# Performance work log

Measured on AMD Instinct MI355X. Metric: run time of the kernel, lower is better.

The kernel has to match this reference:

```python
import jax, jax.numpy as jnp
import numpy as np
from jax import lax

S, B, V, E, H = 512, 64, 50000, 400, 1150


def _lstm_layer(x, h0, c0, Wih, Whh, bih, bhh):
    # x: [S, B, Din]; PyTorch LSTM gate order: i, f, g, o
    WihT, WhhT = Wih.T, Whh.T

    def step(carry, xt):
        h, c = carry
        gates = xt @ WihT + bih + h @ WhhT + bhh  # [B, 4*Dh]
        i, f, g, o = jnp.split(gates, 4, axis=-1)
        c_new = jax.nn.sigmoid(f) * c + jax.nn.sigmoid(i) * jnp.tanh(g)
        h_new = jax.nn.sigmoid(o) * jnp.tanh(c_new)
        return (h_new, c_new), h_new

    (_, _), ys = lax.scan(step, (h0, c0), x)
    return ys  # [S, B, Dh]


def setup_inputs() -> dict:
    key = jax.random.key(0)

    def u(i, shape, s):
        return jax.random.uniform(jax.random.fold_in(key, i), shape, jnp.float32, -s, s)

    inp = {"tokens": jax.random.randint(jax.random.fold_in(key, 0), (S, B), 0, V)}
    inp["emb_w"] = u(1, (V, E), 0.1)  # encoder.weight.uniform_(-0.1, 0.1)
    dims = [(E, H), (H, H), (H, E)]  # (input_size, hidden_size) per layer
    k = 2
    for l, (din, dh) in enumerate(dims):
        s = 1.0 / float(np.sqrt(dh))
        inp[f"Wih{l}"] = u(k, (4 * dh, din), s); k += 1
        inp[f"Whh{l}"] = u(k, (4 * dh, dh), s); k += 1
        inp[f"bih{l}"] = u(k, (4 * dh,), s); k += 1
        inp[f"bhh{l}"] = u(k, (4 * dh,), s); k += 1
        inp[f"h{l}"] = jnp.zeros((B, dh), jnp.float32)
        inp[f"c{l}"] = jnp.zeros((B, dh), jnp.float32)
    return inp


def reference(tokens, emb_w, Wih0, Whh0, bih0, bhh0, Wih1, Whh1, bih1, bhh1,
              Wih2, Whh2, bih2, bhh2, h0, c0, h1, c1, h2, c2):
    # Eval-mode forward: embedding/locked/weight dropouts are identity.
    x = emb_w[tokens]  # [S, B, E]
    x = _lstm_layer(x, h0, c0, Wih0, Whh0, bih0, bhh0)  # [S, B, H]
    x = _lstm_layer(x, h1, c1, Wih1, Whh1, bih1, bhh1)  # [S, B, H]
    x = _lstm_layer(x, h2, c2, Wih2, Whh2, bih2, bhh2)  # [S, B, E]
    return x
```

## Files before the change

kernel.cpp:

```cpp
#include <hip/hip_runtime.h>
#include <hip/hip_bf16.h>
#include <cstdint>
#include <cstddef>


typedef _Float16 f16x8 __attribute__((ext_vector_type(8)));
typedef float f32x4 __attribute__((ext_vector_type(4)));
typedef unsigned int u32x4 __attribute__((ext_vector_type(4)));

#define LSTM_NBLK   241
#define LSTM_WSTEPS 515
#define THREADS     512
#define LDS_W_HALFS (4 * 36 * 64 * 8)
#define LDS_TOTAL_BYTES (LDS_W_HALFS * 2 + 16384)
#define GO_BASE 248

struct KParams {
  const unsigned short* res[3];
  const unsigned short* strm[3];
  const float* bias[3];
  const unsigned short* xin0;
  unsigned short* hseq[3];
  float* part;
  float* out;
  int* bar;
};

__device__ __forceinline__ float sigm_(float x) { return 1.0f / (1.0f + __expf(-x)); }
__device__ __forceinline__ float tanh_(float x) { return 2.0f * sigm_(2.0f * x) - 1.0f; }
__device__ __forceinline__ unsigned short f2h(float x) {
  _Float16 h = (_Float16)x;
  return __builtin_bit_cast(unsigned short, h);
}
__device__ __forceinline__ f32x4 load_sc128f(const float* p) {
  f32x4 r;
  asm volatile("global_load_dwordx4 %0, %1, off sc0 sc1"
               : "=v"(r) : "v"(p) : "memory");
  return r;
}
__device__ __forceinline__ void store_sc128(unsigned short* p, u32x4 v) {
  asm volatile("global_store_dwordx4 %0, %1, off sc0 sc1" :: "v"(p), "v"(v) : "memory");
}
__device__ __forceinline__ void store_sc128f(float* p, f32x4 v) {
  asm volatile("global_store_dwordx4 %0, %1, off sc0 sc1" :: "v"(p), "v"(v) : "memory");
}
__device__ __forceinline__ void store_sc_i(int* p, int v) {
  asm volatile("global_store_dword %0, %1, off sc0 sc1" :: "v"(p), "v"(v) : "memory");
}
__device__ __forceinline__ int load_sc_i(const int* p) {
  int v;
  asm volatile("global_load_dword %0, %1, off sc0 sc1\n\ts_waitcnt vmcnt(0)"
               : "=v"(v) : "v"(p) : "memory");
  __builtin_amdgcn_sched_barrier(0);
  return v;
}
__device__ __forceinline__ void wait_vm0() {
  asm volatile("s_waitcnt vmcnt(0)" ::: "memory");
  __builtin_amdgcn_sched_barrier(0);
}

__device__ __forceinline__ void grid_barrier(int* bar, int bid, int tid, int tau1) {
  wait_vm0();
  __syncthreads();
  if (bid == 0) {
    if (tid >= 1 && tid < LSTM_NBLK) {
      int guard = 0;
      while (load_sc_i(&bar[tid * 32]) < tau1 && ++guard < (1 << 20))
        __builtin_amdgcn_s_sleep(1);
    }
    __syncthreads();
    if (tid < 8) store_sc_i(&bar[(GO_BASE + tid) * 32], tau1);
  } else {
    if (tid == 0) {
      store_sc_i(&bar[bid * 32], tau1);
      int guard = 0;
      while (load_sc_i(&bar[(GO_BASE + (bid & 7)) * 32]) < tau1 && ++guard < (1 << 20))
        __builtin_amdgcn_s_sleep(1);
    }
    __syncthreads();
  }
}

template<bool HASP>
__device__ __forceinline__ float lstm_ew(float* gates, int e, const float b4[4],
                                         const f32x4* pl, float& c_val) {
  float pg[4];
#pragma unroll
  for (int s2 = 0; s2 < 4; ++s2) {
    pg[s2] = gates[s2 * 1024 + e];
    gates[s2 * 1024 + e] = 0.0f;
  }
  float ig = sigm_(pg[0] + (HASP ? (*pl)[0] : 0.0f) + b4[0]);
  float fg = sigm_(pg[1] + (HASP ? (*pl)[1] : 0.0f) + b4[1]);
  float gg = tanh_(pg[2] + (HASP ? (*pl)[2] : 0.0f) + b4[2]);
  float og = sigm_(pg[3] + (HASP ? (*pl)[3] : 0.0f) + b4[3]);
  c_val = fg * c_val + ig * gg;
  return og * tanh_(c_val);
}

__device__ __forceinline__ void pack_store16(unsigned short* base, int lane, float h) {
  unsigned v0  = (unsigned)f2h(h);
  unsigned o1  = __shfl_down(v0, 1);
  unsigned p01 = v0 | (o1 << 16);
  unsigned o2  = __shfl_down(p01, 2);
  unsigned o4a = __shfl_down(p01, 4);
  unsigned o4b = __shfl_down(o2, 4);
  if ((lane & 7) == 0) {
    u32x4 pk; pk[0] = p01; pk[1] = o2; pk[2] = o4a; pk[3] = o4b;
    store_sc128(base, pk);
  }
}

__device__ __forceinline__ void run_l0(const KParams& p, int g, int bid,
                                       unsigned short* ldsW, float* gates) {
  const unsigned short* __restrict__ strmA = p.strm[0] + (size_t)g * (4 * 13 * 512);
  const unsigned short* __restrict__ xin   = p.xin0;
  unsigned short* __restrict__ own         = p.hseq[0];

  const int tid  = threadIdx.x;
  const int lane = tid & 63;
  const int w    = tid >> 6;
  const int kq   = w & 3;
  const int m0   = (w >> 2) * 32;
  const int r    = lane & 15;
  const int q    = lane >> 4;

  {
    const uint4* src = (const uint4*)(p.res[0] + (size_t)g * LDS_W_HALFS);
    uint4* dst = (uint4*)ldsW;
    for (int i = tid; i < LDS_W_HALFS / 8; i += THREADS) dst[i] = src[i];
#pragma unroll
    for (int s2 = 0; s2 < 4; ++s2) {
      gates[s2 * 1024 + tid] = 0.0f;
      gates[s2 * 1024 + tid + 512] = 0.0f;
    }
  }
  const int jp = tid & 15;
  const int jglob = g * 16 + jp;
  float bias4[4];
#pragma unroll
  for (int ss = 0; ss < 4; ++ss) bias4[ss] = p.bias[0][ss * 1152 + jglob];
  float c0 = 0.0f, c1 = 0.0f;
  __syncthreads();

  for (int tau = 0; tau < LSTM_WSTEPS; ++tau) {
    const int t = tau;
    if (t < 512) {
      f16x8 a2r[2][9];
#pragma unroll
      for (int mi = 0; mi < 2; ++mi) {
        const unsigned short* a2b =
            own + (size_t)t * (64 * 1152) + (size_t)(m0 + mi * 16 + r) * 1152 + q * 8;
#pragma unroll
        for (int i = 0; i < 9; ++i) a2r[mi][i] = *(const f16x8*)(a2b + (kq + 4 * i) * 32);
      }
      f16x8 a1r[2][4]; f16x8 bS[4][4];
#pragma unroll
      for (int mi = 0; mi < 2; ++mi) {
        const unsigned short* a1b =
            xin + ((size_t)t * 64 + (m0 + mi * 16 + r)) * 416 + q * 8;
#pragma unroll
        for (int i = 0; i < 4; ++i) {
          int kb = kq + 4 * i;
          if (kb < 13) a1r[mi][i] = *(const f16x8*)(a1b + kb * 32);
        }
      }
#pragma unroll
      for (int i = 0; i < 4; ++i) {
        int kb = kq + 4 * i;
        if (kb < 13) {
#pragma unroll
          for (int s2 = 0; s2 < 4; ++s2)
            bS[i][s2] = *(const f16x8*)&strmA[((size_t)(s2 * 13 + kb) * 64 + lane) * 8];
        }
      }

      f32x4 acc[2][4];
#pragma unroll
      for (int mi = 0; mi < 2; ++mi)
#pragma unroll
        for (int s2 = 0; s2 < 4; ++s2) acc[mi][s2] = (f32x4){0, 0, 0, 0};

#pragma unroll
      for (int i = 0; i < 4; ++i) {
        int kb = kq + 4 * i;
        if (kb < 13) {
#pragma unroll
          for (int s2 = 0; s2 < 4; ++s2)
#pragma unroll
            for (int mi = 0; mi < 2; ++mi)
              acc[mi][s2] = __builtin_amdgcn_mfma_f32_16x16x32_f16(
                  a1r[mi][i], bS[i][s2], acc[mi][s2], 0, 0, 0);
        }
      }
#pragma unroll
      for (int i = 0; i < 9; ++i) {
        int kb = kq + 4 * i;
#pragma unroll
        for (int s2 = 0; s2 < 4; ++s2) {
          f16x8 b = *(const f16x8*)&ldsW[((s2 * 36 + kb) * 64 + lane) * 8];
#pragma unroll
          for (int mi = 0; mi < 2; ++mi)
            acc[mi][s2] = __builtin_amdgcn_mfma_f32_16x16x32_f16(
                a2r[mi][i], b, acc[mi][s2], 0, 0, 0);
        }
      }
#pragma unroll
      for (int mi = 0; mi < 2; ++mi)
#pragma unroll
        for (int s2 = 0; s2 < 4; ++s2)
#pragma unroll
          for (int i = 0; i < 4; ++i)
            atomicAdd(&gates[s2 * 1024 + (m0 + mi * 16 + q * 4 + i) * 16 + r],
                      acc[mi][s2][i]);
      __syncthreads();

      float h0 = lstm_ew<false>(gates, tid, bias4, nullptr, c0);
      float h1 = lstm_ew<false>(gates, tid + 512, bias4, nullptr, c1);
      if (jglob >= 1150) { h0 = 0.0f; h1 = 0.0f; }
      const int b0 = tid >> 4, b1 = b0 + 32;
      pack_store16(own + ((size_t)(t + 1) * 64 + b0) * 1152 + jglob, lane, h0);
      pack_store16(own + ((size_t)(t + 1) * 64 + b1) * 1152 + jglob, lane, h1);
    }
    grid_barrier(p.bar, bid, tid, tau + 1);
  }
}

__device__ __forceinline__ void run_l1_ih(const KParams& p, int g, int bid,
                                          unsigned short* ldsW, float* gates) {
  const unsigned short* __restrict__ xin = p.hseq[0];
  const int tid  = threadIdx.x;
  const int lane = tid & 63;
  const int w    = tid >> 6;
  const int kq   = w & 3;
  const int m0   = (w >> 2) * 32;
  const int r    = lane & 15;
  const int q    = lane >> 4;

  {
    const uint4* src = (const uint4*)(p.strm[1] + (size_t)g * LDS_W_HALFS);
    uint4* dst = (uint4*)ldsW;
    for (int i = tid; i < LDS_W_HALFS / 8; i += THREADS) dst[i] = src[i];
#pragma unroll
    for (int s2 = 0; s2 < 4; ++s2) {
      gates[s2 * 1024 + tid] = 0.0f;
      gates[s2 * 1024 + tid + 512] = 0.0f;
    }
  }
  __syncthreads();

  for (int tau = 0; tau < LSTM_WSTEPS; ++tau) {
    const int t = tau - 1;
    if (t >= 0 && t < 512) {
      f16x8 a1r[2][9];
#pragma unroll
      for (int mi = 0; mi < 2; ++mi) {
        const unsigned short* a1b =
            xin + (size_t)(t + 1) * (64 * 1152) + (size_t)(m0 + mi * 16 + r) * 1152 + q * 8;
#pragma unroll
        for (int i = 0; i < 9; ++i) a1r[mi][i] = *(const f16x8*)(a1b + (kq + 4 * i) * 32);
      }
      f32x4 acc[2][4];
#pragma unroll
      for (int mi = 0; mi < 2; ++mi)
#pragma unroll
        for (int s2 = 0; s2 < 4; ++s2) acc[mi][s2] = (f32x4){0, 0, 0, 0};
#pragma unroll
      for (int i = 0; i < 9; ++i) {
        int kb = kq + 4 * i;
#pragma unroll
        for (int s2 = 0; s2 < 4; ++s2) {
          f16x8 b = *(const f16x8*)&ldsW[((s2 * 36 + kb) * 64 + lane) * 8];
#pragma unroll
          for (int mi = 0; mi < 2; ++mi)
            acc[mi][s2] = __builtin_amdgcn_mfma_f32_16x16x32_f16(
                a1r[mi][i], b, acc[mi][s2], 0, 0, 0);
        }
      }
#pragma unroll
      for (int mi = 0; mi < 2; ++mi)
#pragma unroll
        for (int s2 = 0; s2 < 4; ++s2)
#pragma unroll
          for (int i = 0; i < 4; ++i)
            atomicAdd(&gates[s2 * 1024 + (m0 + mi * 16 + q * 4 + i) * 16 + r],
                      acc[mi][s2][i]);
      __syncthreads();

      f32x4 pk0, pk1;
#pragma unroll
      for (int s2 = 0; s2 < 4; ++s2) {
        pk0[s2] = gates[s2 * 1024 + tid];       gates[s2 * 1024 + tid] = 0.0f;
        pk1[s2] = gates[s2 * 1024 + tid + 512]; gates[s2 * 1024 + tid + 512] = 0.0f;
      }
      float* pb = p.part + (size_t)((t & 1) * 72 + g) * 1024 * 4;
      store_sc128f(pb + (size_t)tid * 4, pk0);
      store_sc128f(pb + (size_t)(tid + 512) * 4, pk1);
    }
    grid_barrier(p.bar, bid, tid, tau + 1);
  }
}

__device__ __forceinline__ void run_l1_hh(const KParams& p, int g, int bid,
                                          unsigned short* ldsW, float* gates) {
  unsigned short* __restrict__ own = p.hseq[1];
  const int tid  = threadIdx.x;
  const int lane = tid & 63;
  const int w    = tid >> 6;
  const int kq   = w & 3;
  const int m0   = (w >> 2) * 32;
  const int r    = lane & 15;
  const int q    = lane >> 4;

  {
    const uint4* src = (const uint4*)(p.res[1] + (size_t)g * LDS_W_HALFS);
    uint4* dst = (uint4*)ldsW;
    for (int i = tid; i < LDS_W_HALFS / 8; i += THREADS) dst[i] = src[i];
#pragma unroll
    for (int s2 = 0; s2 < 4; ++s2) {
      gates[s2 * 1024 + tid] = 0.0f;
      gates[s2 * 1024 + tid + 512] = 0.0f;
    }
  }
  const int jp = tid & 15;
  const int jglob = g * 16 + jp;
  float bias4[4];
#pragma unroll
  for (int ss = 0; ss < 4; ++ss) bias4[ss] = p.bias[1][ss * 1152 + jglob];
  float c0 = 0.0f, c1 = 0.0f;
  __syncthreads();

  for (int tau = 0; tau < LSTM_WSTEPS; ++tau) {
    const int t = tau - 2;
    if (t >= 0 && t < 512) {
      f16x8 a2r[2][9];
#pragma unroll
      for (int mi = 0; mi < 2; ++mi) {
        const unsigned short* a2b =
            own + (size_t)t * (64 * 1152) + (size_t)(m0 + mi * 16 + r) * 1152 + q * 8;
#pragma unroll
        for (int i = 0; i < 9; ++i) a2r[mi][i] = *(const f16x8*)(a2b + (kq + 4 * i) * 32);
      }
      const float* pb = p.part + (size_t)((t & 1) * 72 + g) * 1024 * 4;
      f32x4 pl0 = load_sc128f(pb + (size_t)tid * 4);
      f32x4 pl1 = load_sc128f(pb + (size_t)(tid + 512) * 4);
      wait_vm0();

      f32x4 acc[2][4];
#pragma unroll
      for (int mi = 0; mi < 2; ++mi)
#pragma unroll
        for (int s2 = 0; s2 < 4; ++s2) acc[mi][s2] = (f32x4){0, 0, 0, 0};
#pragma unroll
      for (int i = 0; i < 9; ++i) {
        int kb = kq + 4 * i;
#pragma unroll
        for (int s2 = 0; s2 < 4; ++s2) {
          f16x8 b = *(const f16x8*)&ldsW[((s2 * 36 + kb) * 64 + lane) * 8];
#pragma unroll
          for (int mi = 0; mi < 2; ++mi)
            acc[mi][s2] = __builtin_amdgcn_mfma_f32_16x16x32_f16(
                a2r[mi][i], b, acc[mi][s2], 0, 0, 0);
        }
      }
#pragma unroll
      for (int mi = 0; mi < 2; ++mi)
#pragma unroll
        for (int s2 = 0; s2 < 4; ++s2)
#pragma unroll
          for (int i = 0; i < 4; ++i)
            atomicAdd(&gates[s2 * 1024 + (m0 + mi * 16 + q * 4 + i) * 16 + r],
                      acc[mi][s2][i]);
      __syncthreads();

      float h0 = lstm_ew<true>(gates, tid, bias4, &pl0, c0);
      float h1 = lstm_ew<true>(gates, tid + 512, bias4, &pl1, c1);
      if (jglob >= 1150) { h0 = 0.0f; h1 = 0.0f; }
      const int b0 = tid >> 4, b1 = b0 + 32;
      pack_store16(own + ((size_t)(t + 1) * 64 + b0) * 1152 + jglob, lane, h0);
      pack_store16(own + ((size_t)(t + 1) * 64 + b1) * 1152 + jglob, lane, h1);
    }
    grid_barrier(p.bar, bid, tid, tau + 1);
  }
}

__device__ __forceinline__ void run_l2(const KParams& p, int g, int bid,
                                       unsigned short* ldsW, float* gates) {
  const unsigned short* __restrict__ strmB = p.strm[2] + (size_t)g * (4 * 13 * 512);
  const unsigned short* __restrict__ xin   = p.hseq[1];
  unsigned short* __restrict__ own         = p.hseq[2];

  const int tid  = threadIdx.x;
  const int lane = tid & 63;
  const int w    = tid >> 6;
  const int kq   = w & 3;
  const int m0   = (w >> 2) * 32;
  const int r    = lane & 15;
  const int q    = lane >> 4;

  {
    const uint4* src = (const uint4*)(p.res[2] + (size_t)g * LDS_W_HALFS);
    uint4* dst = (uint4*)ldsW;
    for (int i = tid; i < LDS_W_HALFS / 8; i += THREADS) dst[i] = src[i];
#pragma unroll
    for (int s2 = 0; s2 < 4; ++s2) {
      gates[s2 * 1024 + tid] = 0.0f;
      gates[s2 * 1024 + tid + 512] = 0.0f;
    }
  }
  const int jp = tid & 15;
  const int jglob = g * 16 + jp;
  float bias4[4];
#pragma unroll
  for (int ss = 0; ss < 4; ++ss) bias4[ss] = p.bias[2][ss * 1152 + jglob];
  float c0 = 0.0f, c1 = 0.0f;
  __syncthreads();

  for (int tau = 0; tau < LSTM_WSTEPS; ++tau) {
    const int t = tau - 3;
    if (t >= 0 && t < 512) {
      f16x8 a1r[2][9];
#pragma unroll
      for (int mi = 0; mi < 2; ++mi) {
        const unsigned short* a1b =
            xin + (size_t)(t + 1) * (64 * 1152) + (size_t)(m0 + mi * 16 + r) * 1152 + q * 8;
#pragma unroll
        for (int i = 0; i < 9; ++i) a1r[mi][i] = *(const f16x8*)(a1b + (kq + 4 * i) * 32);
      }
      f16x8 a2r[2][4];
#pragma unroll
      for (int mi = 0; mi < 2; ++mi) {
        const unsigned short* a2b =
            own + (size_t)t * (64 * 416) + (size_t)(m0 + mi * 16 + r) * 416 + q * 8;
#pragma unroll
        for (int i = 0; i < 4; ++i) {
          int kb = kq + 4 * i;
          if (kb < 13) a2r[mi][i] = *(const f16x8*)(a2b + kb * 32);
        }
      }
      f16x8 bS[4][4];
#pragma unroll
      for (int i = 0; i < 4; ++i) {
        int kb = kq + 4 * i;
        if (kb < 13) {
#pragma unroll
          for (int s2 = 0; s2 < 4; ++s2)
            bS[i][s2] = *(const f16x8*)&strmB[((size_t)(s2 * 13 + kb) * 64 + lane) * 8];
        }
      }

      f32x4 acc[2][4];
#pragma unroll
      for (int mi = 0; mi < 2; ++mi)
#pragma unroll
        for (int s2 = 0; s2 < 4; ++s2) acc[mi][s2] = (f32x4){0, 0, 0, 0};

#pragma unroll
      for (int i = 0; i < 9; ++i) {
        int kb = kq + 4 * i;
#pragma unroll
        for (int s2 = 0; s2 < 4; ++s2) {
          f16x8 b = *(const f16x8*)&ldsW[((s2 * 36 + kb) * 64 + lane) * 8];
#pragma unroll
          for (int mi = 0; mi < 2; ++mi)
            acc[mi][s2] = __builtin_amdgcn_mfma_f32_16x16x32_f16(
                a1r[mi][i], b, acc[mi][s2], 0, 0, 0);
        }
      }
#pragma unroll
      for (int i = 0; i < 4; ++i) {
        int kb = kq + 4 * i;
        if (kb < 13) {
#pragma unroll
          for (int s2 = 0; s2 < 4; ++s2)
#pragma unroll
            for (int mi = 0; mi < 2; ++mi)
              acc[mi][s2] = __builtin_amdgcn_mfma_f32_16x16x32_f16(
                  a2r[mi][i], bS[i][s2], acc[mi][s2], 0, 0, 0);
        }
      }
#pragma unroll
      for (int mi = 0; mi < 2; ++mi)
#pragma unroll
        for (int s2 = 0; s2 < 4; ++s2)
#pragma unroll
          for (int i = 0; i < 4; ++i)
            atomicAdd(&gates[s2 * 1024 + (m0 + mi * 16 + q * 4 + i) * 16 + r],
                      acc[mi][s2][i]);
      __syncthreads();

      float h0 = lstm_ew<false>(gates, tid, bias4, nullptr, c0);
      float h1 = lstm_ew<false>(gates, tid + 512, bias4, nullptr, c1);
      if (jglob >= 400) { h0 = 0.0f; h1 = 0.0f; }
      const int b0 = tid >> 4, b1 = b0 + 32;
      pack_store16(own + ((size_t)(t + 1) * 64 + b0) * 416 + jglob, lane, h0);
      pack_store16(own + ((size_t)(t + 1) * 64 + b1) * 416 + jglob, lane, h1);
      if (jglob < 400) {
        p.out[((size_t)t * 64 + b0) * 400 + jglob] = h0;
        p.out[((size_t)t * 64 + b1) * 400 + jglob] = h1;
      }
    }
    grid_barrier(p.bar, bid, tid, tau + 1);
  }
}

__global__ void __launch_bounds__(THREADS, 2) lstm_persistent(KParams p) {
  extern __shared__ unsigned short smem[];
  unsigned short* ldsW = smem;
  float* gates = (float*)(smem + LDS_W_HALFS);
  const int bid = blockIdx.x;
  if (bid < 72)       run_l0(p, bid, bid, ldsW, gates);
  else if (bid < 144) run_l1_ih(p, bid - 72, bid, ldsW, gates);
  else if (bid < 216) run_l1_hh(p, bid - 144, bid, ldsW, gates);
  else                run_l2(p, bid - 216, bid, ldsW, gates);
}

__global__ void prep_weights(const float* __restrict__ src,
                             unsigned short* __restrict__ dst,
                             int Jext, int jg, int K, int NKB) {
  const int n = jg * 4 * NKB * 512;
  for (int idx = blockIdx.x * blockDim.x + threadIdx.x; idx < n;
       idx += gridDim.x * blockDim.x) {
    int e = idx & 7;
    int t2 = idx >> 3;
    int ln = t2 & 63; t2 >>= 6;
    int kb = t2 % NKB; t2 /= NKB;
    int s = t2 & 3;
    int g = t2 >> 2;
    int j = g * 16 + (ln & 15);
    int k = kb * 32 + (ln >> 4) * 8 + e;
    unsigned short v = 0;
    if (j < Jext && k < K) v = f2h(src[(size_t)(s * Jext + j) * K + k]);
    dst[idx] = v;
  }
}

__global__ void prep_bias(const float* __restrict__ bih,
                          const float* __restrict__ bhh,
                          float* __restrict__ dst, int Dh) {
  const int n = 4 * 1152;
  for (int idx = blockIdx.x * blockDim.x + threadIdx.x; idx < n;
       idx += gridDim.x * blockDim.x) {
    int s = idx / 1152, j = idx % 1152;
    float v = 0.0f;
    if (j < Dh) v = bih[s * Dh + j] + bhh[s * Dh + j];
    dst[idx] = v;
  }
}

__global__ void prep_gather(const int* __restrict__ tokens,
                            const float* __restrict__ emb,
                            unsigned short* __restrict__ xin0) {
  const int n = 512 * 64 * 52;
  for (int idx = blockIdx.x * blockDim.x + threadIdx.x; idx < n;
       idx += gridDim.x * blockDim.x) {
    int row = idx / 52;
    int cp  = idx - row * 52;
    unsigned short v[8] = {0, 0, 0, 0, 0, 0, 0, 0};
    if (cp < 50) {
      const float* src = emb + (size_t)tokens[row] * 400 + cp * 8;
      float4 a = *(const float4*)(src);
      float4 b = *(const float4*)(src + 4);
      v[0] = f2h(a.x); v[1] = f2h(a.y); v[2] = f2h(a.z); v[3] = f2h(a.w);
      v[4] = f2h(b.x); v[5] = f2h(b.y); v[6] = f2h(b.z); v[7] = f2h(b.w);
    }
    *(uint4*)(xin0 + (size_t)row * 416 + cp * 8) = *(const uint4*)v;
  }
}

extern "C" void kernel_launch(void* const* d_in, const int* in_sizes, int n_in,
                              void* d_out, int out_size, void* d_ws, size_t ws_size,
                              hipStream_t stream) {
  const int*   tokens = (const int*)d_in[0];
  const float* emb  = (const float*)d_in[1];
  const float* Wih0 = (const float*)d_in[2];
  const float* Whh0 = (const float*)d_in[3];
  const float* bih0 = (const float*)d_in[4];
  const float* bhh0 = (const float*)d_in[5];
  const float* Wih1 = (const float*)d_in[8];
  const float* Whh1 = (const float*)d_in[9];
  const float* bih1 = (const float*)d_in[10];
  const float* bhh1 = (const float*)d_in[11];
  const float* Wih2 = (const float*)d_in[14];
  const float* Whh2 = (const float*)d_in[15];
  const float* bih2 = (const float*)d_in[16];
  const float* bhh2 = (const float*)d_in[17];

  char* ws = (char*)d_ws;
  size_t off = 0;
  auto alloc = [&](size_t bytes) -> char* {
    char* ptr = ws + off;
    off += (bytes + 255) & ~(size_t)255;
    return ptr;
  };
  unsigned short* res0  = (unsigned short*)alloc(72ull * 4 * 36 * 512 * 2);
  unsigned short* res1  = (unsigned short*)alloc(72ull * 4 * 36 * 512 * 2);
  unsigned short* res2  = (unsigned short*)alloc(25ull * 4 * 36 * 512 * 2);
  unsigned short* strm0 = (unsigned short*)alloc(72ull * 4 * 13 * 512 * 2);
  unsigned short* strm1 = (unsigned short*)alloc(72ull * 4 * 36 * 512 * 2);
  unsigned short* strm2 = (unsigned short*)alloc(25ull * 4 * 13 * 512 * 2);
  float* bias0 = (float*)alloc(4ull * 1152 * 4);
  float* bias1 = (float*)alloc(4ull * 1152 * 4);
  float* bias2 = (float*)alloc(4ull * 1152 * 4);
  unsigned short* xin0  = (unsigned short*)alloc(512ull * 64 * 416 * 2);
  unsigned short* hseq0 = (unsigned short*)alloc(513ull * 64 * 1152 * 2);
  unsigned short* hseq1 = (unsigned short*)alloc(513ull * 64 * 1152 * 2);
  unsigned short* hseq2 = (unsigned short*)alloc(513ull * 64 * 416 * 2);
  float* part = (float*)alloc(2ull * 72 * 1024 * 4 * 4);
  int* bar = (int*)alloc((GO_BASE + 8) * 32 * 4);
  if (off > ws_size) return;

  hipLaunchKernelGGL(prep_gather, dim3(2048), dim3(256), 0, stream, tokens, emb, xin0);
  hipLaunchKernelGGL(prep_weights, dim3(4096), dim3(256), 0, stream, Whh0, res0, 1150, 72, 1150, 36);
  hipLaunchKernelGGL(prep_weights, dim3(4096), dim3(256), 0, stream, Whh1, res1, 1150, 72, 1150, 36);
  hipLaunchKernelGGL(prep_weights, dim3(4096), dim3(256), 0, stream, Wih2, res2, 400, 25, 1150, 36);
  hipLaunchKernelGGL(prep_weights, dim3(4096), dim3(256), 0, stream, Wih0, strm0, 1150, 72, 400, 13);
  hipLaunchKernelGGL(prep_weights, dim3(4096), dim3(256), 0, stream, Wih1, strm1, 1150, 72, 1150, 36);
  hipLaunchKernelGGL(prep_weights, dim3(4096), dim3(256), 0, stream, Whh2, strm2, 400, 25, 400, 13);
  hipLaunchKernelGGL(prep_bias, dim3(8), dim3(256), 0, stream, bih0, bhh0, bias0, 1150);
  hipLaunchKernelGGL(prep_bias, dim3(8), dim3(256), 0, stream, bih1, bhh1, bias1, 1150);
  hipLaunchKernelGGL(prep_bias, dim3(8), dim3(256), 0, stream, bih2, bhh2, bias2, 400);
  (void)hipMemsetAsync(hseq0, 0, 64ull * 1152 * 2, stream);
  (void)hipMemsetAsync(hseq1, 0, 64ull * 1152 * 2, stream);
  (void)hipMemsetAsync(hseq2, 0, 64ull * 416 * 2, stream);
  (void)hipMemsetAsync(bar, 0, (GO_BASE + 8) * 32 * 4, stream);

  KParams kp;
  kp.res[0] = res0;  kp.res[1] = res1;  kp.res[2] = res2;
  kp.strm[0] = strm0; kp.strm[1] = strm1; kp.strm[2] = strm2;
  kp.bias[0] = bias0; kp.bias[1] = bias1; kp.bias[2] = bias2;
  kp.xin0 = xin0;
  kp.hseq[0] = hseq0; kp.hseq[1] = hseq1; kp.hseq[2] = hseq2;
  kp.part = part;
  kp.out = (float*)d_out;
  kp.bar = bar;

  (void)hipFuncSetAttribute((const void*)lstm_persistent,
                            hipFuncAttributeMaxDynamicSharedMemorySize,
                            LDS_TOTAL_BYTES);
  hipLaunchKernelGGL(lstm_persistent, dim3(LSTM_NBLK), dim3(THREADS),
                     LDS_TOTAL_BYTES, stream, kp);
}
```

Baseline: 16.02 ms.

## Replace global grid barrier with per-group dataflow flags and deeper partial buffer

Replaces the single grid-wide barrier that lock-stepped all four block groups (layer0, layer1-ih, layer1-hh, layer2) with per-group barriers plus per-group 'go' flags. Each group waits only on the producers it depends on, so groups can run ahead of each other in a wavefront. The partial-gate ring buffer is deepened to 8 slots so the layer1 input projection can run up to 7 steps ahead of its consumer. Cross-block activation loads now bypass the cache via sc0/sc1 loads, which adds some load latency and more flag-polling traffic.

After: 16.70 ms. +4.3%, slower.

```diff
diff --git a/kernel.cpp b/kernel.cpp
--- a/kernel.cpp
+++ b/kernel.cpp
@@ -9,10 +9,10 @@
 typedef unsigned int u32x4 __attribute__((ext_vector_type(4)));
 
 #define LSTM_NBLK   241
-#define LSTM_WSTEPS 515
 #define THREADS     512
 #define LDS_W_HALFS (4 * 36 * 64 * 8)
 #define LDS_TOTAL_BYTES (LDS_W_HALFS * 2 + 16384)
+#define PDEPTH 8
 #define GO_BASE 248
 
 struct KParams {
@@ -32,6 +32,12 @@
   _Float16 h = (_Float16)x;
   return __builtin_bit_cast(unsigned short, h);
 }
+__device__ __forceinline__ u32x4 load_sc(const unsigned short* p) {
+  u32x4 r;
+  asm volatile("global_load_dwordx4 %0, %1, off sc0 sc1"
+               : "=v"(r) : "v"(p) : "memory");
+  return r;
+}
 __device__ __forceinline__ f32x4 load_sc128f(const float* p) {
   f32x4 r;
   asm volatile("global_load_dwordx4 %0, %1, off sc0 sc1"
@@ -59,25 +65,27 @@
   __builtin_amdgcn_sched_barrier(0);
 }
 
-__device__ __forceinline__ void grid_barrier(int* bar, int bid, int tid, int tau1) {
+__device__ __forceinline__ void spin_ge(const int* p, int th) {
+  int guard = 0;
+  while (load_sc_i(p) < th && ++guard < (1 << 20))
+    __builtin_amdgcn_s_sleep(2);
+}
+__device__ __forceinline__ void wait_go2(int* bar, int tid, int bid,
+                                         int grpA, int thA, int grpB, int thB) {
+  if (thA > 0 && tid == 0)   spin_ge(&bar[(GO_BASE + grpA * 8 + (bid & 7)) * 32], thA);
+  if (thB > 0 && tid == 256) spin_ge(&bar[(GO_BASE + grpB * 8 + (bid & 7)) * 32], thB);
+  __syncthreads();
+}
+__device__ __forceinline__ void finish_step(int* bar, int bid, int tid,
+                                            int gbase, int gsize, int grp, int tau1) {
   wait_vm0();
   __syncthreads();
-  if (bid == 0) {
-    if (tid >= 1 && tid < LSTM_NBLK) {
-      int guard = 0;
-      while (load_sc_i(&bar[tid * 32]) < tau1 && ++guard < (1 << 20))
-        __builtin_amdgcn_s_sleep(1);
-    }
+  if (bid == gbase) {
+    if (tid >= 1 && tid < gsize) spin_ge(&bar[(gbase + tid) * 32], tau1);
     __syncthreads();
-    if (tid < 8) store_sc_i(&bar[(GO_BASE + tid) * 32], tau1);
+    if (tid < 8) store_sc_i(&bar[(GO_BASE + grp * 8 + tid) * 32], tau1);
   } else {
-    if (tid == 0) {
-      store_sc_i(&bar[bid * 32], tau1);
-      int guard = 0;
-      while (load_sc_i(&bar[(GO_BASE + (bid & 7)) * 32]) < tau1 && ++guard < (1 << 20))
-        __builtin_amdgcn_s_sleep(1);
-    }
-    __syncthreads();
+    if (tid == 0) store_sc_i(&bar[bid * 32], tau1);
   }
 }
 
@@ -143,86 +151,87 @@
   float c0 = 0.0f, c1 = 0.0f;
   __syncthreads();
 
-  for (int tau = 0; tau < LSTM_WSTEPS; ++tau) {
-    const int t = tau;
-    if (t < 512) {
-      f16x8 a2r[2][9];
-#pragma unroll
-      for (int mi = 0; mi < 2; ++mi) {
-        const unsigned short* a2b =
-            own + (size_t)t * (64 * 1152) + (size_t)(m0 + mi * 16 + r) * 1152 + q * 8;
-#pragma unroll
-        for (int i = 0; i < 9; ++i) a2r[mi][i] = *(const f16x8*)(a2b + (kq + 4 * i) * 32);
-      }
-      f16x8 a1r[2][4]; f16x8 bS[4][4];
-#pragma unroll
-      for (int mi = 0; mi < 2; ++mi) {
-        const unsigned short* a1b =
-            xin + ((size_t)t * 64 + (m0 + mi * 16 + r)) * 416 + q * 8;
-#pragma unroll
-        for (int i = 0; i < 4; ++i) {
-          int kb = kq + 4 * i;
-          if (kb < 13) a1r[mi][i] = *(const f16x8*)(a1b + kb * 32);
-        }
-      }
+  for (int t = 0; t < 512; ++t) {
+    wait_go2(p.bar, tid, bid, 0, t, 0, 0);
+
+    u32x4 a2r[2][9];
+#pragma unroll
+    for (int mi = 0; mi < 2; ++mi) {
+      const unsigned short* a2b =
+          own + (size_t)t * (64 * 1152) + (size_t)(m0 + mi * 16 + r) * 1152 + q * 8;
+#pragma unroll
+      for (int i = 0; i < 9; ++i) a2r[mi][i] = load_sc(a2b + (kq + 4 * i) * 32);
+    }
+    f16x8 a1r[2][4]; f16x8 bS[4][4];
+#pragma unroll
+    for (int mi = 0; mi < 2; ++mi) {
+      const unsigned short* a1b =
+          xin + ((size_t)t * 64 + (m0 + mi * 16 + r)) * 416 + q * 8;
 #pragma unroll
       for (int i = 0; i < 4; ++i) {
         int kb = kq + 4 * i;
-        if (kb < 13) {
-#pragma unroll
-          for (int s2 = 0; s2 < 4; ++s2)
-            bS[i][s2] = *(const f16x8*)&strmA[((size_t)(s2 * 13 + kb) * 64 + lane) * 8];
-        }
-      }
-
-      f32x4 acc[2][4];
-#pragma unroll
-      for (int mi = 0; mi < 2; ++mi)
-#pragma unroll
-        for (int s2 = 0; s2 < 4; ++s2) acc[mi][s2] = (f32x4){0, 0, 0, 0};
-
-#pragma unroll
-      for (int i = 0; i < 4; ++i) {
-        int kb = kq + 4 * i;
-        if (kb < 13) {
-#pragma unroll
-          for (int s2 = 0; s2 < 4; ++s2)
-#pragma unroll
-            for (int mi = 0; mi < 2; ++mi)
-              acc[mi][s2] = __builtin_amdgcn_mfma_f32_16x16x32_f16(
-                  a1r[mi][i], bS[i][s2], acc[mi][s2], 0, 0, 0);
-        }
-      }
-#pragma unroll
-      for (int i = 0; i < 9; ++i) {
-        int kb = kq + 4 * i;
-#pragma unroll
-        for (int s2 = 0; s2 < 4; ++s2) {
-          f16x8 b = *(const f16x8*)&ldsW[((s2 * 36 + kb) * 64 + lane) * 8];
+        if (kb < 13) a1r[mi][i] = *(const f16x8*)(a1b + kb * 32);
+      }
+    }
+#pragma unroll
+    for (int i = 0; i < 4; ++i) {
+      int kb = kq + 4 * i;
+      if (kb < 13) {
+#pragma unroll
+        for (int s2 = 0; s2 < 4; ++s2)
+          bS[i][s2] = *(const f16x8*)&strmA[((size_t)(s2 * 13 + kb) * 64 + lane) * 8];
+      }
+    }
+    wait_vm0();
+
+    f32x4 acc[2][4];
+#pragma unroll
+    for (int mi = 0; mi < 2; ++mi)
+#pragma unroll
+      for (int s2 = 0; s2 < 4; ++s2) acc[mi][s2] = (f32x4){0, 0, 0, 0};
+
+#pragma unroll
+    for (int i = 0; i < 4; ++i) {
+      int kb = kq + 4 * i;
+      if (kb < 13) {
+#pragma unroll
+        for (int s2 = 0; s2 < 4; ++s2)
 #pragma unroll
           for (int mi = 0; mi < 2; ++mi)
             acc[mi][s2] = __builtin_amdgcn_mfma_f32_16x16x32_f16(
-                a2r[mi][i], b, acc[mi][s2], 0, 0, 0);
-        }
-      }
-#pragma unroll
-      for (int mi = 0; mi < 2; ++mi)
-#pragma unroll
-        for (int s2 = 0; s2 < 4; ++s2)
-#pragma unroll
-          for (int i = 0; i < 4; ++i)
-            atomicAdd(&gates[s2 * 1024 + (m0 + mi * 16 + q * 4 + i) * 16 + r],
-                      acc[mi][s2][i]);
-      __syncthreads();
-
-      float h0 = lstm_ew<false>(gates, tid, bias4, nullptr, c0);
-      float h1 = lstm_ew<false>(gates, tid + 512, bias4, nullptr, c1);
-      if (jglob >= 1150) { h0 = 0.0f; h1 = 0.0f; }
-      const int b0 = tid >> 4, b1 = b0 + 32;
-      pack_store16(own + ((size_t)(t + 1) * 64 + b0) * 1152 + jglob, lane, h0);
-      pack_store16(own + ((size_t)(t + 1) * 64 + b1) * 1152 + jglob, lane, h1);
-    }
-    grid_barrier(p.bar, bid, tid, tau + 1);
+                a1r[mi][i], bS[i][s2], acc[mi][s2], 0, 0, 0);
+      }
+    }
+#pragma unroll
+    for (int i = 0; i < 9; ++i) {
+      int kb = kq + 4 * i;
+#pragma unroll
+      for (int s2 = 0; s2 < 4; ++s2) {
+        f16x8 b = *(const f16x8*)&ldsW[((s2 * 36 + kb) * 64 + lane) * 8];
+#pragma unroll
+        for (int mi = 0; mi < 2; ++mi)
+          acc[mi][s2] = __builtin_amdgcn_mfma_f32_16x16x32_f16(
+              __builtin_bit_cast(f16x8, a2r[mi][i]), b, acc[mi][s2], 0, 0, 0);
+      }
+    }
+#pragma unroll
+    for (int mi = 0; mi < 2; ++mi)
+#pragma unroll
+      for (int s2 = 0; s2 < 4; ++s2)
+#pragma unroll
+        for (int i = 0; i < 4; ++i)
+          atomicAdd(&gates[s2 * 1024 + (m0 + mi * 16 + q * 4 + i) * 16 + r],
+                    acc[mi][s2][i]);
+    __syncthreads();
+
+    float h0 = lstm_ew<false>(gates, tid, bias4, nullptr, c0);
+    float h1 = lstm_ew<false>(gates, tid + 512, bias4, nullptr, c1);
+    if (jglob >= 1150) { h0 = 0.0f; h1 = 0.0f; }
+    const int b0 = tid >> 4, b1 = b0 + 32;
+    pack_store16(own + ((size_t)(t + 1) * 64 + b0) * 1152 + jglob, lane, h0);
+    pack_store16(own + ((size_t)(t + 1) * 64 + b1) * 1152 + jglob, lane, h1);
+
+    finish_step(p.bar, bid, tid, 0, 72, 0, t + 1);
   }
 }
 
@@ -249,55 +258,57 @@
   }
   __syncthreads();
 
-  for (int tau = 0; tau < LSTM_WSTEPS; ++tau) {
-    const int t = tau - 1;
-    if (t >= 0 && t < 512) {
-      f16x8 a1r[2][9];
-#pragma unroll
-      for (int mi = 0; mi < 2; ++mi) {
-        const unsigned short* a1b =
-            xin + (size_t)(t + 1) * (64 * 1152) + (size_t)(m0 + mi * 16 + r) * 1152 + q * 8;
-#pragma unroll
-        for (int i = 0; i < 9; ++i) a1r[mi][i] = *(const f16x8*)(a1b + (kq + 4 * i) * 32);
-      }
-      f32x4 acc[2][4];
-#pragma unroll
-      for (int mi = 0; mi < 2; ++mi)
-#pragma unroll
-        for (int s2 = 0; s2 < 4; ++s2) acc[mi][s2] = (f32x4){0, 0, 0, 0};
-#pragma unroll
-      for (int i = 0; i < 9; ++i) {
-        int kb = kq + 4 * i;
-#pragma unroll
-        for (int s2 = 0; s2 < 4; ++s2) {
-          f16x8 b = *(const f16x8*)&ldsW[((s2 * 36 + kb) * 64 + lane) * 8];
-#pragma unroll
-          for (int mi = 0; mi < 2; ++mi)
-            acc[mi][s2] = __builtin_amdgcn_mfma_f32_16x16x32_f16(
-                a1r[mi][i], b, acc[mi][s2], 0, 0, 0);
-        }
-      }
-#pragma unroll
-      for (int mi = 0; mi < 2; ++mi)
-#pragma unroll
-        for (int s2 = 0; s2 < 4; ++s2)
-#pragma unroll
-          for (int i = 0; i < 4; ++i)
-            atomicAdd(&gates[s2 * 1024 + (m0 + mi * 16 + q * 4 + i) * 16 + r],
-                      acc[mi][s2][i]);
-      __syncthreads();
-
-      f32x4 pk0, pk1;
+  for (int t = 0; t < 512; ++t) {
+    wait_go2(p.bar, tid, bid, 0, t + 1, 2, t - (PDEPTH - 1));
+
+    u32x4 a1r[2][9];
+#pragma unroll
+    for (int mi = 0; mi < 2; ++mi) {
+      const unsigned short* a1b =
+          xin + (size_t)(t + 1) * (64 * 1152) + (size_t)(m0 + mi * 16 + r) * 1152 + q * 8;
+#pragma unroll
+      for (int i = 0; i < 9; ++i) a1r[mi][i] = load_sc(a1b + (kq + 4 * i) * 32);
+    }
+    wait_vm0();
+
+    f32x4 acc[2][4];
+#pragma unroll
+    for (int mi = 0; mi < 2; ++mi)
+#pragma unroll
+      for (int s2 = 0; s2 < 4; ++s2) acc[mi][s2] = (f32x4){0, 0, 0, 0};
+#pragma unroll
+    for (int i = 0; i < 9; ++i) {
+      int kb = kq + 4 * i;
 #pragma unroll
       for (int s2 = 0; s2 < 4; ++s2) {
-        pk0[s2] = gates[s2 * 1024 + tid];       gates[s2 * 1024 + tid] = 0.0f;
-        pk1[s2] = gates[s2 * 1024 + tid + 512]; gates[s2 * 1024 + tid + 512] = 0.0f;
-      }
-      float* pb = p.part + (size_t)((t & 1) * 72 + g) * 1024 * 4;
-      store_sc128f(pb + (size_t)tid * 4, pk0);
-      store_sc128f(pb + (size_t)(tid + 512) * 4, pk1);
-    }
-    grid_barrier(p.bar, bid, tid, tau + 1);
+        f16x8 b = *(const f16x8*)&ldsW[((s2 * 36 + kb) * 64 + lane) * 8];
+#pragma unroll
+        for (int mi = 0; mi < 2; ++mi)
+          acc[mi][s2] = __builtin_amdgcn_mfma_f32_16x16x32_f16(
+              __builtin_bit_cast(f16x8, a1r[mi][i]), b, acc[mi][s2], 0, 0, 0);
+      }
+    }
+#pragma unroll
+    for (int mi = 0; mi < 2; ++mi)
+#pragma unroll
+      for (int s2 = 0; s2 < 4; ++s2)
+#pragma unroll
+        for (int i = 0; i < 4; ++i)
+          atomicAdd(&gates[s2 * 1024 + (m0 + mi * 16 + q * 4 + i) * 16 + r],
+                    acc[mi][s2][i]);
+    __syncthreads();
+
+    f32x4 pk0, pk1;
+#pragma unroll
+    for (int s2 = 0; s2 < 4; ++s2) {
+      pk0[s2] = gates[s2 * 1024 + tid];       gates[s2 * 1024 + tid] = 0.0f;
+      pk1[s2] = gates[s2 * 1024 + tid + 512]; gates[s2 * 1024 + tid + 512] = 0.0f;
+    }
+    float* pb = p.part + (size_t)((t & (PDEPTH - 1)) * 72 + g) * 1024 * 4;
+    store_sc128f(pb + (size_t)tid * 4, pk0);
+    store_sc128f(pb + (size_t)(tid + 512) * 4, pk1);
+
+    finish_step(p.bar, bid, tid, 72, 72, 1, t + 1);
   }
 }
 
@@ -330,57 +341,57 @@
   float c0 = 0.0f, c1 = 0.0f;
   __syncthreads();
 
-  for (int tau = 0; tau < LSTM_WSTEPS; ++tau) {
-    const int t = tau - 2;
-    if (t >= 0 && t < 512) {
-      f16x8 a2r[2][9];
-#pragma unroll
-      for (int mi = 0; mi < 2; ++mi) {
-        const unsigned short* a2b =
-            own + (size_t)t * (64 * 1152) + (size_t)(m0 + mi * 16 + r) * 1152 + q * 8;
-#pragma unroll
-        for (int i = 0; i < 9; ++i) a2r[mi][i] = *(const f16x8*)(a2b + (kq + 4 * i) * 32);
-      }
-      const float* pb = p.part + (size_t)((t & 1) * 72 + g) * 1024 * 4;
-      f32x4 pl0 = load_sc128f(pb + (size_t)tid * 4);
-      f32x4 pl1 = load_sc128f(pb + (size_t)(tid + 512) * 4);
-      wait_vm0();
-
-      f32x4 acc[2][4];
-#pragma unroll
-      for (int mi = 0; mi < 2; ++mi)
-#pragma unroll
-        for (int s2 = 0; s2 < 4; ++s2) acc[mi][s2] = (f32x4){0, 0, 0, 0};
-#pragma unroll
-      for (int i = 0; i < 9; ++i) {
-        int kb = kq + 4 * i;
-#pragma unroll
-        for (int s2 = 0; s2 < 4; ++s2) {
-          f16x8 b = *(const f16x8*)&ldsW[((s2 * 36 + kb) * 64 + lane) * 8];
-#pragma unroll
-          for (int mi = 0; mi < 2; ++mi)
-            acc[mi][s2] = __builtin_amdgcn_mfma_f32_16x16x32_f16(
-                a2r[mi][i], b, acc[mi][s2], 0, 0, 0);
-        }
-      }
-#pragma unroll
-      for (int mi = 0; mi < 2; ++mi)
-#pragma unroll
-        for (int s2 = 0; s2 < 4; ++s2)
-#pragma unroll
-          for (int i = 0; i < 4; ++i)
-            atomicAdd(&gates[s2 * 1024 + (m0 + mi * 16 + q * 4 + i) * 16 + r],
-                      acc[mi][s2][i]);
-      __syncthreads();
-
-      float h0 = lstm_ew<true>(gates, tid, bias4, &pl0, c0);
-      float h1 = lstm_ew<true>(gates, tid + 512, bias4, &pl1, c1);
-      if (jglob >= 1150) { h0 = 0.0f; h1 = 0.0f; }
-      const int b0 = tid >> 4, b1 = b0 + 32;
-      pack_store16(own + ((size_t)(t + 1) * 64 + b0) * 1152 + jglob, lane, h0);
-      pack_store16(own + ((size_t)(t + 1) * 64 + b1) * 1152 + jglob, lane, h1);
-    }
-    grid_barrier(p.bar, bid, tid, tau + 1);
+  for (int t = 0; t < 512; ++t) {
+    wait_go2(p.bar, tid, bid, 1, t + 1, 2, t);
+
+    u32x4 a2r[2][9];
+#pragma unroll
+    for (int mi = 0; mi < 2; ++mi) {
+      const unsigned short* a2b =
+          own + (size_t)t * (64 * 1152) + (size_t)(m0 + mi * 16 + r) * 1152 + q * 8;
+#pragma unroll
+      for (int i = 0; i < 9; ++i) a2r[mi][i] = load_sc(a2b + (kq + 4 * i) * 32);
+    }
+    const float* pb = p.part + (size_t)((t & (PDEPTH - 1)) * 72 + g) * 1024 * 4;
+    f32x4 pl0 = load_sc128f(pb + (size_t)tid * 4);
+    f32x4 pl1 = load_sc128f(pb + (size_t)(tid + 512) * 4);
+    wait_vm0();
+
+    f32x4 acc[2][4];
+#pragma unroll
+    for (int mi = 0; mi < 2; ++mi)
+#pragma unroll
+      for (int s2 = 0; s2 < 4; ++s2) acc[mi][s2] = (f32x4){0, 0, 0, 0};
+#pragma unroll
+    for (int i = 0; i < 9; ++i) {
+      int kb = kq + 4 * i;
+#pragma unroll
+      for (int s2 = 0; s2 < 4; ++s2) {
+        f16x8 b = *(const f16x8*)&ldsW[((s2 * 36 + kb) * 64 + lane) * 8];
+#pragma unroll
+        for (int mi = 0; mi < 2; ++mi)
+          acc[mi][s2] = __builtin_amdgcn_mfma_f32_16x16x32_f16(
+              __builtin_bit_cast(f16x8, a2r[mi][i]), b, acc[mi][s2], 0, 0, 0);
+      }
+    }
+#pragma unroll
+    for (int mi = 0; mi < 2; ++mi)
+#pragma unroll
+      for (int s2 = 0; s2 < 4; ++s2)
+#pragma unroll
+        for (int i = 0; i < 4; ++i)
+          atomicAdd(&gates[s2 * 1024 + (m0 + mi * 16 + q * 4 + i) * 16 + r],
+                    acc[mi][s2][i]);
+    __syncthreads();
+
+    float h0 = lstm_ew<true>(gates, tid, bias4, &pl0, c0);
+    float h1 = lstm_ew<true>(gates, tid + 512, bias4, &pl1, c1);
+    if (jglob >= 1150) { h0 = 0.0f; h1 = 0.0f; }
+    const int b0 = tid >> 4, b1 = b0 + 32;
+    pack_store16(own + ((size_t)(t + 1) * 64 + b0) * 1152 + jglob, lane, h0);
+    pack_store16(own + ((size_t)(t + 1) * 64 + b1) * 1152 + jglob, lane, h1);
+
+    finish_step(p.bar, bid, tid, 144, 72, 2, t + 1);
   }
 }
 
@@ -416,91 +427,92 @@
   float c0 = 0.0f, c1 = 0.0f;
   __syncthreads();
 
-  for (int tau = 0; tau < LSTM_WSTEPS; ++tau) {
-    const int t = tau - 3;
-    if (t >= 0 && t < 512) {
-      f16x8 a1r[2][9];
-#pragma unroll
-      for (int mi = 0; mi < 2; ++mi) {
-        const unsigned short* a1b =
-            xin + (size_t)(t + 1) * (64 * 1152) + (size_t)(m0 + mi * 16 + r) * 1152 + q * 8;
-#pragma unroll
-        for (int i = 0; i < 9; ++i) a1r[mi][i] = *(const f16x8*)(a1b + (kq + 4 * i) * 32);
-      }
-      f16x8 a2r[2][4];
-#pragma unroll
-      for (int mi = 0; mi < 2; ++mi) {
-        const unsigned short* a2b =
-            own + (size_t)t * (64 * 416) + (size_t)(m0 + mi * 16 + r) * 416 + q * 8;
-#pragma unroll
-        for (int i = 0; i < 4; ++i) {
-          int kb = kq + 4 * i;
-          if (kb < 13) a2r[mi][i] = *(const f16x8*)(a2b + kb * 32);
-        }
-      }
-      f16x8 bS[4][4];
+  for (int t = 0; t < 512; ++t) {
+    wait_go2(p.bar, tid, bid, 2, t + 1, 3, t);
+
+    u32x4 a1r[2][9];
+#pragma unroll
+    for (int mi = 0; mi < 2; ++mi) {
+      const unsigned short* a1b =
+          xin + (size_t)(t + 1) * (64 * 1152) + (size_t)(m0 + mi * 16 + r) * 1152 + q * 8;
+#pragma unroll
+      for (int i = 0; i < 9; ++i) a1r[mi][i] = load_sc(a1b + (kq + 4 * i) * 32);
+    }
+    u32x4 a2r[2][4];
+#pragma unroll
+    for (int mi = 0; mi < 2; ++mi) {
+      const unsigned short* a2b =
+          own + (size_t)t * (64 * 416) + (size_t)(m0 + mi * 16 + r) * 416 + q * 8;
 #pragma unroll
       for (int i = 0; i < 4; ++i) {
         int kb = kq + 4 * i;
-        if (kb < 13) {
-#pragma unroll
-          for (int s2 = 0; s2 < 4; ++s2)
-            bS[i][s2] = *(const f16x8*)&strmB[((size_t)(s2 * 13 + kb) * 64 + lane) * 8];
-        }
-      }
-
-      f32x4 acc[2][4];
-#pragma unroll
-      for (int mi = 0; mi < 2; ++mi)
-#pragma unroll
-        for (int s2 = 0; s2 < 4; ++s2) acc[mi][s2] = (f32x4){0, 0, 0, 0};
-
-#pragma unroll
-      for (int i = 0; i < 9; ++i) {
-        int kb = kq + 4 * i;
-#pragma unroll
-        for (int s2 = 0; s2 < 4; ++s2) {
-          f16x8 b = *(const f16x8*)&ldsW[((s2 * 36 + kb) * 64 + lane) * 8];
+        if (kb < 13) a2r[mi][i] = load_sc(a2b + kb * 32);
+      }
+    }
+    f16x8 bS[4][4];
+#pragma unroll
+    for (int i = 0; i < 4; ++i) {
+      int kb = kq + 4 * i;
+      if (kb < 13) {
+#pragma unroll
+        for (int s2 = 0; s2 < 4; ++s2)
+          bS[i][s2] = *(const f16x8*)&strmB[((size_t)(s2 * 13 + kb) * 64 + lane) * 8];
+      }
+    }
+    wait_vm0();
+
+    f32x4 acc[2][4];
+#pragma unroll
+    for (int mi = 0; mi < 2; ++mi)
+#pragma unroll
+      for (int s2 = 0; s2 < 4; ++s2) acc[mi][s2] = (f32x4){0, 0, 0, 0};
+
+#pragma unroll
+    for (int i = 0; i < 9; ++i) {
+      int kb = kq + 4 * i;
+#pragma unroll
+      for (int s2 = 0; s2 < 4; ++s2) {
+        f16x8 b = *(const f16x8*)&ldsW[((s2 * 36 + kb) * 64 + lane) * 8];
+#pragma unroll
+        for (int mi = 0; mi < 2; ++mi)
+          acc[mi][s2] = __builtin_amdgcn_mfma_f32_16x16x32_f16(
+              __builtin_bit_cast(f16x8, a1r[mi][i]), b, acc[mi][s2], 0, 0, 0);
+      }
+    }
+#pragma unroll
+    for (int i = 0; i < 4; ++i) {
+      int kb = kq + 4 * i;
+      if (kb < 13) {
+#pragma unroll
+        for (int s2 = 0; s2 < 4; ++s2)
 #pragma unroll
           for (int mi = 0; mi < 2; ++mi)
             acc[mi][s2] = __builtin_amdgcn_mfma_f32_16x16x32_f16(
-                a1r[mi][i], b, acc[mi][s2], 0, 0, 0);
-        }
-      }
-#pragma unroll
-      for (int i = 0; i < 4; ++i) {
-        int kb = kq + 4 * i;
-        if (kb < 13) {
-#pragma unroll
-          for (int s2 = 0; s2 < 4; ++s2)
-#pragma unroll
-            for (int mi = 0; mi < 2; ++mi)
-              acc[mi][s2] = __builtin_amdgcn_mfma_f32_16x16x32_f16(
-                  a2r[mi][i], bS[i][s2], acc[mi][s2], 0, 0, 0);
-        }
-      }
-#pragma unroll
-      for (int mi = 0; mi < 2; ++mi)
-#pragma unroll
-        for (int s2 = 0; s2 < 4; ++s2)
-#pragma unroll
-          for (int i = 0; i < 4; ++i)
-            atomicAdd(&gates[s2 * 1024 + (m0 + mi * 16 + q * 4 + i) * 16 + r],
-                      acc[mi][s2][i]);
-      __syncthreads();
-
-      float h0 = lstm_ew<false>(gates, tid, bias4, nullptr, c0);
-      float h1 = lstm_ew<false>(gates, tid + 512, bias4, nullptr, c1);
-      if (jglob >= 400) { h0 = 0.0f; h1 = 0.0f; }
-      const int b0 = tid >> 4, b1 = b0 + 32;
-      pack_store16(own + ((size_t)(t + 1) * 64 + b0) * 416 + jglob, lane, h0);
-      pack_store16(own + ((size_t)(t + 1) * 64 + b1) * 416 + jglob, lane, h1);
-      if (jglob < 400) {
-        p.out[((size_t)t * 64 + b0) * 400 + jglob] = h0;
-        p.out[((size_t)t * 64 + b1) * 400 + jglob] = h1;
-      }
-    }
-    grid_barrier(p.bar, bid, tid, tau + 1);
+                __builtin_bit_cast(f16x8, a2r[mi][i]), bS[i][s2], acc[mi][s2], 0, 0, 0);
+      }
+    }
+#pragma unroll
+    for (int mi = 0; mi < 2; ++mi)
+#pragma unroll
+      for (int s2 = 0; s2 < 4; ++s2)
+#pragma unroll
+        for (int i = 0; i < 4; ++i)
+          atomicAdd(&gates[s2 * 1024 + (m0 + mi * 16 + q * 4 + i) * 16 + r],
+                    acc[mi][s2][i]);
+    __syncthreads();
+
+    float h0 = lstm_ew<false>(gates, tid, bias4, nullptr, c0);
+    float h1 = lstm_ew<false>(gates, tid + 512, bias4, nullptr, c1);
+    if (jglob >= 400) { h0 = 0.0f; h1 = 0.0f; }
+    const int b0 = tid >> 4, b1 = b0 + 32;
+    pack_store16(own + ((size_t)(t + 1) * 64 + b0) * 416 + jglob, lane, h0);
+    pack_store16(own + ((size_t)(t + 1) * 64 + b1) * 416 + jglob, lane, h1);
+    if (jglob < 400) {
+      p.out[((size_t)t * 64 + b0) * 400 + jglob] = h0;
+      p.out[((size_t)t * 64 + b1) * 400 + jglob] = h1;
+    }
+
+    finish_step(p.bar, bid, tid, 216, 25, 3, t + 1);
   }
 }
 
@@ -606,8 +618,8 @@
   unsigned short* hseq0 = (unsigned short*)alloc(513ull * 64 * 1152 * 2);
   unsigned short* hseq1 = (unsigned short*)alloc(513ull * 64 * 1152 * 2);
   unsigned short* hseq2 = (unsigned short*)alloc(513ull * 64 * 416 * 2);
-  float* part = (float*)alloc(2ull * 72 * 1024 * 4 * 4);
-  int* bar = (int*)alloc((GO_BASE + 8) * 32 * 4);
+  float* part = (float*)alloc((size_t)PDEPTH * 72 * 1024 * 4 * 4);
+  int* bar = (int*)alloc((GO_BASE + 32) * 32 * 4);
   if (off > ws_size) return;
 
   hipLaunchKernelGGL(prep_gather, dim3(2048), dim3(256), 0, stream, tokens, emb, xin0);
@@ -623,7 +635,7 @@
   (void)hipMemsetAsync(hseq0, 0, 64ull * 1152 * 2, stream);
   (void)hipMemsetAsync(hseq1, 0, 64ull * 1152 * 2, stream);
   (void)hipMemsetAsync(hseq2, 0, 64ull * 416 * 2, stream);
-  (void)hipMemsetAsync(bar, 0, (GO_BASE + 8) * 32 * 4, stream);
+  (void)hipMemsetAsync(bar, 0, (GO_BASE + 32) * 32 * 4, stream);
 
   KParams kp;
   kp.res[0] = res0;  kp.res[1] = res1;  kp.res[2] = res2;
```
